# Performance work log

Measured on AMD Instinct MI355X. Metric: run time of the kernel, lower is better.

The kernel has to match this reference:

```python
import jax, jax.numpy as jnp
import numpy as np

K = 49        # k_neighbors
EPS = 1e-5    # BatchNorm2d eps


def setup_inputs() -> dict:
    key = jax.random.key(0)
    ks = jax.random.split(key, 2)
    B, C, M, O = 64, 64, 32, 128
    X = jax.random.normal(ks[0], (B, C, M, M), dtype=jnp.float32)
    # conv1x1 weight (kaiming fan_out) flattened to (O, C); bias init 0
    W = jax.random.normal(ks[1], (O, C), dtype=jnp.float32) * (2.0 / O) ** 0.5
    b = jnp.zeros((O,), jnp.float32)
    gamma = jnp.ones((O,), jnp.float32)
    beta = jnp.zeros((O,), jnp.float32)
    run_mean = jnp.zeros((O,), jnp.float32)
    run_var = jnp.ones((O,), jnp.float32)
    return dict(X=X, W=W, b=b, gamma=gamma, beta=beta,
                run_mean=run_mean, run_var=run_var)


def _knn_aggregate(x):
    """x: (N, C) node features -> D^{-1/2} A D^{-1/2} x for the kNN graph."""
    N = x.shape[0]
    sq = jnp.sum(x * x, axis=1)
    d2 = sq[:, None] + sq[None, :] - 2.0 * (x @ x.T)
    dist = jnp.sqrt(jnp.maximum(d2, 0.0))              # torch.cdist (p=2)
    i = jnp.arange(N)
    dist = dist.at[i, i].set(jnp.inf)                  # fill_diagonal_(inf)
    _, knn = jax.lax.top_k(-dist, K)                   # (N, K) nearest indices
    # topk indices are distinct -> every row degree == K, and the column
    # normalizer uses the col node's row degree (also K), so
    # D^{-1/2} A D^{-1/2} x == mean of gathered neighbors.
    nb = x[knn]                                        # (N, K, C) gather
    return nb.sum(axis=1) / K


def reference(X, W, b, gamma, beta, run_mean, run_var):
    B, C, M, _ = X.shape
    N = M * M
    x = X.reshape(B, C, N).transpose(0, 2, 1)          # (B, N, C) nodes
    Z = jax.vmap(_knn_aggregate)(x)                    # (B, N, C) sparse GCN agg
    # 1x1 conv over the (M, M) grid == per-node linear map
    Fg = jnp.einsum('oc,bnc->bon', W, Z) + b[None, :, None]   # (B, O, N)
    Fg = jax.nn.relu(Fg)
    # BatchNorm2d with running stats (eval mode); Dropout2d is identity in eval
    inv = jax.lax.rsqrt(run_var + EPS)
    Fg = gamma[None, :, None] * (Fg - run_mean[None, :, None]) * inv[None, :, None] + beta[None, :, None]
    return Fg.mean(axis=2)                             # AdaptiveAvgPool2d(1) -> (B, O)
```

## Files before the change

kernel.cpp:

```cpp
#include <hip/hip_runtime.h>
#include <stdint.h>

#define BATCH 64
#define CDIM  64
#define NPTS  1024
#define ODIM  128
#define KNN   49
#define KNNP  52
#define BNEPS 1e-5f
#define ZPAD  72

typedef __attribute__((ext_vector_type(8))) short bf16x8;
typedef __attribute__((ext_vector_type(4))) float f32x4;
typedef union { bf16x8 v; uint32_t d[4]; } bfu;

__device__ __forceinline__ int mbcnt64(unsigned long long m) {
    return __builtin_amdgcn_mbcnt_hi((uint32_t)(m >> 32),
           __builtin_amdgcn_mbcnt_lo((uint32_t)m, 0));
}

__device__ __forceinline__ void bf16_split(float x, uint32_t& h, uint32_t& l) {
    uint32_t u = __float_as_uint(x);
    h = (u + 0x7FFFu + ((u >> 16) & 1u)) >> 16;
    float hf = __uint_as_float(h << 16);
    uint32_t ul = __float_as_uint(x - hf);
    l = (ul + 0x7FFFu + ((ul >> 16) & 1u)) >> 16;
}

#define O_XF   0
#define SZ_XF  (BATCH*64*2*64*8*4)
#define O_SQ   (O_XF + SZ_XF)
#define SZ_SQ  (BATCH*NPTS*4)
#define O_WF   (O_SQ + SZ_SQ)
#define SZ_WF  (2*16*64*16)
#define O_BM   (O_WF + SZ_WF)
#define SZ_BM  (BATCH*NPTS*32*4)
#define O_XFT  (O_BM + SZ_BM)
#define SZ_XFT (BATCH*32*4*64*8*4)
#define WS_NEED ((size_t)(O_XFT + SZ_XFT))

__global__ void gcn_init(const float* __restrict__ gamma, const float* __restrict__ beta,
                         const float* __restrict__ rmean, const float* __restrict__ rvar,
                         float* __restrict__ out) {
    int i = blockIdx.x * 256 + threadIdx.x;
    if (i < BATCH * ODIM) {
        int o = i & (ODIM - 1);
        out[i] = beta[o] - gamma[o] * rmean[o] * rsqrtf(rvar[o] + BNEPS);
    }
}

__global__ __launch_bounds__(256) void k0_split(const float* __restrict__ X,
                                                const float* __restrict__ W,
                                                uint32_t* __restrict__ XF,
                                                float* __restrict__ sq,
                                                uint32_t* __restrict__ XFT,
                                                uint32_t* __restrict__ WFh,
                                                uint32_t* __restrict__ WFl,
                                                const float* __restrict__ gamma,
                                                const float* __restrict__ beta,
                                                const float* __restrict__ rmean,
                                                const float* __restrict__ rvar,
                                                float* __restrict__ out) {
    if (blockIdx.x < 32) {
        int i = blockIdx.x * 256 + threadIdx.x;
        int o = i & (ODIM - 1);
        out[i] = beta[o] - gamma[o] * rmean[o] * rsqrtf(rvar[o] + BNEPS);
    } else if (blockIdx.x < 36) {
        int item = (blockIdx.x - 32) * 256 + threadIdx.x;
        int e = item >> 6, ln = item & 63;
        int nt = e >> 1, kt = e & 1;
        int o = nt * 16 + (ln & 15);
        int kc = kt * 32 + (ln >> 4) * 8;
        const float* wp = W + (size_t)o * CDIM + kc;
        uint32_t h[8], l[8];
#pragma unroll
        for (int jj = 0; jj < 8; jj++) bf16_split(wp[jj], h[jj], l[jj]);
        *(uint4*)&WFh[item * 4] = make_uint4(h[0] | (h[1] << 16), h[2] | (h[3] << 16),
                                             h[4] | (h[5] << 16), h[6] | (h[7] << 16));
        *(uint4*)&WFl[item * 4] = make_uint4(l[0] | (l[1] << 16), l[2] | (l[3] << 16),
                                             l[4] | (l[5] << 16), l[6] | (l[7] << 16));
    }
    const int b    = blockIdx.x >> 4;
    const int g    = blockIdx.x & 15;
    const int wv   = threadIdx.x >> 6;
    const int t16  = g * 4 + wv;
    const int lane = threadIdx.x & 63;
    const int n    = t16 * 16 + (lane & 15);
    const int cg   = lane >> 4;
    const float* Xb = X + (size_t)b * CDIM * NPTS;
    float s = 0.f;
    for (int ks = 0; ks < 2; ks++) {
        uint32_t hi[4], lo[4];
#pragma unroll
        for (int dj = 0; dj < 4; dj++) {
            uint32_t hw[2], lw[2];
#pragma unroll
            for (int e = 0; e < 2; e++) {
                int c = ks * 32 + cg * 8 + dj * 2 + e;
                float x = Xb[(size_t)c * NPTS + n];
                s += x * x;
                bf16_split(x, hw[e], lw[e]);
            }
            hi[dj] = hw[0] | (hw[1] << 16);
            lo[dj] = lw[0] | (lw[1] << 16);
        }
        size_t entry = ((size_t)(b * 64 + t16) * 2 + ks) * 64 + lane;
        uint32_t* p = XF + entry * 8;
        *(uint4*)p       = make_uint4(hi[0], hi[1], hi[2], hi[3]);
        *(uint4*)(p + 4) = make_uint4(lo[0], lo[1], lo[2], lo[3]);
    }
    s += __shfl_xor(s, 16, 64);
    s += __shfl_xor(s, 32, 64);
    if (lane < 16) sq[b * NPTS + n] = s;

#pragma unroll
    for (int sx = 0; sx < 2; sx++) {
        int task = g * 8 + wv * 2 + sx;
        int kt = task >> 2, ct = task & 3;
        int c  = ct * 16 + (lane & 15);
        int n0 = kt * 32 + (lane >> 4) * 8;
        const float* xp = Xb + (size_t)c * NPTS + n0;
        uint32_t h[8], l[8];
#pragma unroll
        for (int j = 0; j < 8; j++) bf16_split(xp[j], h[j], l[j]);
        uint32_t* pp = XFT + ((((size_t)b * 32 + kt) * 4 + ct) * 64 + lane) * 8;
        *(uint4*)pp       = make_uint4(h[0] | (h[1] << 16), h[2] | (h[3] << 16),
                                       h[4] | (h[5] << 16), h[6] | (h[7] << 16));
        *(uint4*)(pp + 4) = make_uint4(l[0] | (l[1] << 16), l[2] | (l[3] << 16),
                                       l[4] | (l[5] << 16), l[6] | (l[7] << 16));
    }
}

__global__ __launch_bounds__(512, 6) void k1_gram_select(const uint32_t* __restrict__ XF,
                                                         const float* __restrict__ sq,
                                                         uint32_t* __restrict__ BM) {
    __shared__ uint32_t s_pk[8 * 1024];
    __shared__ uint32_t s_bm[16][32];
    const int b    = blockIdx.x >> 6;
    const int rt   = blockIdx.x & 63;
    const int wave = threadIdx.x >> 6, lane = threadIdx.x & 63;
    const int q = lane >> 4, l15 = lane & 15;

    bf16x8 ahi[2], alo[2];
#pragma unroll
    for (int ks = 0; ks < 2; ks++) {
        const uint32_t* p = XF + (((size_t)(b * 64 + rt) * 2 + ks) * 64 + lane) * 8;
        ahi[ks] = *(const bf16x8*)p;
        alo[ks] = *(const bf16x8*)(p + 4);
    }
    const float* sqb = sq + b * NPTS;

#pragma unroll
    for (int tt = 0; tt < 8; tt++) {
        const int t16 = wave * 8 + tt;
        f32x4 acc = {0.f, 0.f, 0.f, 0.f};
#pragma unroll
        for (int ks = 0; ks < 2; ks++) {
            const uint32_t* p = XF + (((size_t)(b * 64 + t16) * 2 + ks) * 64 + lane) * 8;
            bf16x8 bhi = *(const bf16x8*)p;
            bf16x8 blo = *(const bf16x8*)(p + 4);
            acc = __builtin_amdgcn_mfma_f32_16x16x32_bf16(ahi[ks], bhi, acc, 0, 0, 0);
            acc = __builtin_amdgcn_mfma_f32_16x16x32_bf16(alo[ks], bhi, acc, 0, 0, 0);
            acc = __builtin_amdgcn_mfma_f32_16x16x32_bf16(ahi[ks], blo, acc, 0, 0, 0);
        }
        const int col  = t16 * 16 + l15;
        const float sqv = sqb[col];
        uint32_t k16[4];
#pragma unroll
        for (int i = 0; i < 4; i++) {
            int row = q * 4 + i;
            float d = fmaf(-2.f, acc[i], sqv);
            if (col == rt * 16 + row) d = __uint_as_float(0x7F800000u);
            uint32_t u = __float_as_uint(d);
            uint32_t key = ((int)u < 0) ? ~u : (u | 0x80000000u);
            k16[i] = key >> 16;
        }
        const int p0 = 2 * q, p1 = 2 * q + 1;
        s_pk[p0 * 1024 + (col ^ ((p0 & 3) << 3))] = k16[0] | (k16[1] << 16);
        s_pk[p1 * 1024 + (col ^ ((p1 & 3) << 3))] = k16[2] | (k16[3] << 16);
    }
    __syncthreads();

    uint32_t k0r[16], k1r[16];
    {
        const int sw = (wave & 3) << 3;
#pragma unroll
        for (int tt = 0; tt < 16; tt++) {
            uint32_t pk = s_pk[wave * 1024 + ((tt * 64 + lane) ^ sw)];
            k0r[tt] = pk & 0xFFFFu;
            k1r[tt] = pk >> 16;
        }
    }

    uint32_t lo0, hi0, lo1, hi1;
    {
        uint32_t lm0 = k0r[0], lm1 = k1r[0];
#pragma unroll
        for (int tt = 1; tt < 16; tt++) {
            lm0 = k0r[tt] < lm0 ? k0r[tt] : lm0;
            lm1 = k1r[tt] < lm1 ? k1r[tt] : lm1;
        }
        uint32_t g0 = lm0, m0 = lm0, g1 = lm1, m1 = lm1;
#pragma unroll
        for (int off = 1; off < 64; off <<= 1) {
            uint32_t a0 = (uint32_t)__shfl_xor((int)g0, off, 64);
            uint32_t b0 = (uint32_t)__shfl_xor((int)m0, off, 64);
            uint32_t a1 = (uint32_t)__shfl_xor((int)g1, off, 64);
            uint32_t b1 = (uint32_t)__shfl_xor((int)m1, off, 64);
            g0 = a0 < g0 ? a0 : g0;  m0 = b0 > m0 ? b0 : m0;
            g1 = a1 < g1 ? a1 : g1;  m1 = b1 > m1 ? b1 : m1;
        }
        lo0 = g0; hi0 = m0;
        lo1 = g1; hi1 = m1;
    }

    for (int it = 0; it < 16; it++) {
        bool a0 = lo0 < hi0, a1 = lo1 < hi1;
        if (!a0 && !a1) break;
        uint32_t mid0 = (lo0 + hi0) >> 1;
        uint32_t mid1 = (lo1 + hi1) >> 1;
        int cnt0 = 0, cnt1 = 0;
#pragma unroll
        for (int tt = 0; tt < 16; tt++) {
            cnt0 += __popcll(__ballot(k0r[tt] <= mid0));
            cnt1 += __popcll(__ballot(k1r[tt] <= mid1));
        }
        if (a0) { if (cnt0 >= KNN) hi0 = mid0; else lo0 = mid0 + 1; }
        if (a1) { if (cnt1 >= KNN) hi1 = mid1; else lo1 = mid1 + 1; }
    }

#pragma unroll
    for (int r = 0; r < 2; r++) {
        const int row = wave * 2 + r;
        const uint32_t vstar = r ? lo1 : lo0;
        const uint32_t* k = r ? k1r : k0r;
        int total_lt = 0;
#pragma unroll
        for (int tt = 0; tt < 16; tt++)
            total_lt += __popcll(__ballot(k[tt] < vstar));
        int base_eq = total_lt;
#pragma unroll
        for (int tt = 0; tt < 16; tt++) {
            bool islt = k[tt] < vstar;
            bool iseq = k[tt] == vstar;
            unsigned long long meq = __ballot(iseq);
            int pos = base_eq + mbcnt64(meq);
            bool sel = islt || (iseq && pos < KNN);
            unsigned long long msel = __ballot(sel);
            if (lane < 2)
                s_bm[row][tt * 2 + lane] = lane ? (uint32_t)(msel >> 32) : (uint32_t)msel;
            base_eq += __popcll(meq);
        }
    }
    __syncthreads();
    if (threadIdx.x < 128) {
        uint32_t* dst = BM + ((size_t)(b * NPTS + rt * 16) * 32);
        *(uint4*)&dst[threadIdx.x * 4] = *(const uint4*)&((const uint32_t*)s_bm)[threadIdx.x * 4];
    }
}

__global__ __launch_bounds__(256) void k2_agg(const uint32_t* __restrict__ XFT,
                                              const uint32_t* __restrict__ BM,
                                              const uint32_t* __restrict__ WFh,
                                              const uint32_t* __restrict__ WFl,
                                              const float* __restrict__ bias,
                                              const float* __restrict__ gamma,
                                              const float* __restrict__ rvar,
                                              float* __restrict__ out) {
    __shared__ uint32_t bmp[128 * 33];
    __shared__ __align__(16) uint16_t ZFh[128 * ZPAD];
    __shared__ __align__(16) uint16_t ZFl[128 * ZPAD];
    __shared__ float red[512];
    const int b = blockIdx.x >> 3, nq = blockIdx.x & 7;
    const int t = threadIdx.x;
    const int wave = t >> 6, lane = t & 63;
    const int q = lane >> 4, l15 = lane & 15;

    {
        const uint32_t* src = BM + ((size_t)(b * NPTS + nq * 128) * 32);
#pragma unroll
        for (int kk = 0; kk < 16; kk++) {
            int idx = kk * 256 + t;
            uint32_t v = src[idx];
            bmp[(idx >> 5) * 33 + (idx & 31)] = v;
        }
    }
    __syncthreads();

    const int ct = wave;
    f32x4 acc[8];
#pragma unroll
    for (int mt = 0; mt < 8; mt++) acc[mt] = (f32x4){0.f, 0.f, 0.f, 0.f};
    for (int kt = 0; kt < 32; kt++) {
        const uint32_t* p = XFT + ((((size_t)b * 32 + kt) * 4 + ct) * 64 + lane) * 8;
        bf16x8 bhi = *(const bf16x8*)p;
        bf16x8 blo = *(const bf16x8*)(p + 4);
#pragma unroll
        for (int mt = 0; mt < 8; mt++) {
            uint32_t byte = (bmp[(mt * 16 + l15) * 33 + kt] >> (q * 8)) & 0xFFu;
            bfu a;
            a.d[0] = ((byte & 1u)  ? 0x3F80u : 0u) | ((byte & 2u)   ? 0x3F800000u : 0u);
            a.d[1] = ((byte & 4u)  ? 0x3F80u : 0u) | ((byte & 8u)   ? 0x3F800000u : 0u);
            a.d[2] = ((byte & 16u) ? 0x3F80u : 0u) | ((byte & 32u)  ? 0x3F800000u : 0u);
            a.d[3] = ((byte & 64u) ? 0x3F80u : 0u) | ((byte & 128u) ? 0x3F800000u : 0u);
            acc[mt] = __builtin_amdgcn_mfma_f32_16x16x32_bf16(a.v, bhi, acc[mt], 0, 0, 0);
            acc[mt] = __builtin_amdgcn_mfma_f32_16x16x32_bf16(a.v, blo, acc[mt], 0, 0, 0);
        }
    }

#pragma unroll
    for (int mt = 0; mt < 8; mt++) {
#pragma unroll
        for (int reg = 0; reg < 4; reg++) {
            int r = mt * 16 + q * 4 + reg;
            int c = ct * 16 + l15;
            uint32_t h, l;
            bf16_split(acc[mt][reg], h, l);
            ZFh[r * ZPAD + c] = (uint16_t)h;
            ZFl[r * ZPAD + c] = (uint16_t)l;
        }
    }
    __syncthreads();

    bf16x8 zah[2][2], zal[2][2];
#pragma unroll
    for (int m2 = 0; m2 < 2; m2++) {
        const int m = (wave * 2 + m2) * 16 + l15;
#pragma unroll
        for (int kt = 0; kt < 2; kt++) {
            const int kb = kt * 32 + q * 8;
            zah[m2][kt] = *(const bf16x8*)&ZFh[m * ZPAD + kb];
            zal[m2][kt] = *(const bf16x8*)&ZFl[m * ZPAD + kb];
        }
    }
    const float inv49 = 1.f / KNN;
    float p[8];
#pragma unroll
    for (int nt = 0; nt < 8; nt++) {
        const int o = nt * 16 + l15;
        bfu wh[2], wl[2];
#pragma unroll
        for (int kt = 0; kt < 2; kt++) {
            const int item = (nt * 2 + kt) * 64 + lane;
            *(uint4*)wh[kt].d = *(const uint4*)&WFh[item * 4];
            *(uint4*)wl[kt].d = *(const uint4*)&WFl[item * 4];
        }
        f32x4 acc0 = {0.f, 0.f, 0.f, 0.f};
        f32x4 acc1 = {0.f, 0.f, 0.f, 0.f};
#pragma unroll
        for (int kt = 0; kt < 2; kt++) {
            acc0 = __builtin_amdgcn_mfma_f32_16x16x32_bf16(zah[0][kt], wh[kt].v, acc0, 0, 0, 0);
            acc0 = __builtin_amdgcn_mfma_f32_16x16x32_bf16(zal[0][kt], wh[kt].v, acc0, 0, 0, 0);
            acc0 = __builtin_amdgcn_mfma_f32_16x16x32_bf16(zah[0][kt], wl[kt].v, acc0, 0, 0, 0);
            acc1 = __builtin_amdgcn_mfma_f32_16x16x32_bf16(zah[1][kt], wh[kt].v, acc1, 0, 0, 0);
            acc1 = __builtin_amdgcn_mfma_f32_16x16x32_bf16(zal[1][kt], wh[kt].v, acc1, 0, 0, 0);
            acc1 = __builtin_amdgcn_mfma_f32_16x16x32_bf16(zah[1][kt], wl[kt].v, acc1, 0, 0, 0);
        }
        const float bo = bias[o];
        float s = 0.f;
#pragma unroll
        for (int reg = 0; reg < 4; reg++) {
            s += fmaxf(fmaf(acc0[reg], inv49, bo), 0.f);
            s += fmaxf(fmaf(acc1[reg], inv49, bo), 0.f);
        }
        p[nt] = s;
    }
#pragma unroll
    for (int nt = 0; nt < 8; nt++) {
        p[nt] += __shfl_xor(p[nt], 16, 64);
        p[nt] += __shfl_xor(p[nt], 32, 64);
    }
    if (lane < 16) {
#pragma unroll
        for (int nt = 0; nt < 8; nt++)
            red[wave * 128 + nt * 16 + l15] = p[nt];
    }
    __syncthreads();
    if (t < 128) {
        float s = red[t] + red[128 + t] + red[256 + t] + red[384 + t];
        float scale = gamma[t] * rsqrtf(rvar[t] + BNEPS) * (1.f / NPTS);
        atomicAdd(&out[b * ODIM + t], s * scale);
    }
}

#define RTILE 8
#define APAD  1028
#define WPAD  132
#define POOLF (64 * WPAD)

__global__ __launch_bounds__(256) void gcn_main(
    const float* __restrict__ X, const float* __restrict__ W,
    const float* __restrict__ bias, const float* __restrict__ gamma,
    const float* __restrict__ rvar, float* __restrict__ out)
{
    __shared__ __align__(16) float s_pool[POOLF];
    __shared__ __align__(16) float s_fstage[4][APAD];
    __shared__ int   s_knn[RTILE][KNN];
    __shared__ float s_z[RTILE][CDIM];

    const int t = threadIdx.x;
    const int b = blockIdx.x >> 7;
    const int rtile = blockIdx.x & 127;
    const int r0 = rtile * RTILE;
    const float* Xb = X + (size_t)b * CDIM * NPTS;

    float acc[RTILE][4];
    float sqv[4];
#pragma unroll
    for (int r = 0; r < RTILE; r++)
#pragma unroll
        for (int u = 0; u < 4; u++) acc[r][u] = 0.f;
#pragma unroll
    for (int u = 0; u < 4; u++) sqv[u] = 0.f;

    for (int ch = 0; ch < 16; ch++) {
        const int c0 = ch * 4;
#pragma unroll
        for (int cc = 0; cc < 4; cc++) {
            float4 v = *(const float4*)(Xb + (size_t)(c0 + cc) * NPTS + 4 * t);
            *(float4*)&s_fstage[cc][4 * t] = v;
        }
        __syncthreads();
#pragma unroll
        for (int cc = 0; cc < 4; cc++) {
            float4 bv4 = *(const float4*)&s_fstage[cc][4 * t];
            float bv[4] = {bv4.x, bv4.y, bv4.z, bv4.w};
#pragma unroll
            for (int u = 0; u < 4; u++) sqv[u] += bv[u] * bv[u];
            const float* arow = Xb + (size_t)(c0 + cc) * NPTS + r0;
            float4 a0 = *(const float4*)(arow);
            float4 a1 = *(const float4*)(arow + 4);
            float av[8] = {a0.x, a0.y, a0.z, a0.w, a1.x, a1.y, a1.z, a1.w};
#pragma unroll
            for (int r = 0; r < RTILE; r++)
#pragma unroll
                for (int u = 0; u < 4; u++) acc[r][u] += av[r] * bv[u];
        }
        __syncthreads();
    }

    float* s_dist = s_pool;
#pragma unroll
    for (int r = 0; r < RTILE; r++) {
        const int rG = r0 + r;
        float d[4];
#pragma unroll
        for (int u = 0; u < 4; u++) {
            float dd = sqv[u] - 2.f * acc[r][u];
            d[u] = (4 * t + u == rG) ? __uint_as_float(0x7F800000u) : dd;
        }
        *(float4*)&s_dist[r * NPTS + 4 * t] = make_float4(d[0], d[1], d[2], d[3]);
    }
    __syncthreads();

    const int wave = t >> 6, lane = t & 63;
    const unsigned long long ltmask = (1ull << lane) - 1ull;
    for (int rr = 0; rr < 2; rr++) {
        const int row = wave * 2 + rr;
        unsigned key[16];
#pragma unroll
        for (int tt = 0; tt < 16; tt++) {
            unsigned u = __float_as_uint(s_dist[row * NPTS + tt * 64 + lane]);
            key[tt] = (u & 0x80000000u) ? ~u : (u | 0x80000000u);
        }
        unsigned lo = 0u, hi = 0xFFFFFFFFu;
        while (lo < hi) {
            unsigned mid = lo + ((hi - lo) >> 1);
            int cnt = 0;
#pragma unroll
            for (int tt = 0; tt < 16; tt++)
                cnt += __popcll(__ballot(key[tt] <= mid));
            if (cnt >= KNN) hi = mid; else lo = mid + 1;
        }
        const unsigned v49 = lo;
        int cntless = 0;
#pragma unroll
        for (int tt = 0; tt < 16; tt++)
            cntless += __popcll(__ballot(key[tt] < v49));
        const int need = KNN - cntless;
        int base = 0, eqtaken = 0;
#pragma unroll
        for (int tt = 0; tt < 16; tt++) {
            bool islt = key[tt] < v49;
            bool iseq = key[tt] == v49;
            unsigned long long meq = __ballot(iseq);
            int eqrank = eqtaken + __popcll(meq & ltmask);
            bool sel = islt || (iseq && (eqrank < need));
            unsigned long long msel = __ballot(sel);
            if (sel) {
                int pos = base + __popcll(msel & ltmask);
                s_knn[row][pos] = tt * 64 + lane;
            }
            base    += __popcll(msel);
            eqtaken += __popcll(meq);
        }
    }
    __syncthreads();

    float* astage = s_pool;
    float* s_redf = (float*)s_fstage;
    const int ar = t >> 5, acc8 = (t & 31) >> 2, ks = t & 3;
    for (int c0 = 0; c0 < CDIM; c0 += 8) {
#pragma unroll
        for (int qq = 0; qq < 8; qq++) {
            int if4 = qq * 256 + t;
            int cc = if4 >> 8, j4 = if4 & 255;
            float4 v = *(const float4*)(Xb + (size_t)(c0 + cc) * NPTS + 4 * j4);
            *(float4*)&astage[cc * APAD + 4 * j4] = v;
        }
        __syncthreads();
        float partial = 0.f;
        for (int k = ks; k < KNN; k += 4)
            partial += astage[acc8 * APAD + s_knn[ar][k]];
        s_redf[t] = partial;
        __syncthreads();
        if (t < 64) {
            int r = t >> 3, cc = t & 7;
            int bi = r * 32 + cc * 4;
            s_z[r][c0 + cc] = s_redf[bi] + s_redf[bi + 1] + s_redf[bi + 2] + s_redf[bi + 3];
        }
        __syncthreads();
    }

    float* wt = s_pool;
#pragma unroll 4
    for (int qq = 0; qq < 32; qq++) {
        int e = qq * 256 + t;
        int o = e >> 6, c = e & 63;
        wt[c * WPAD + o] = W[e];
    }
    __syncthreads();
    const int o = t & 127, rg = t >> 7;
    float facc[4] = {0.f, 0.f, 0.f, 0.f};
    for (int c = 0; c < CDIM; c += 4) {
        float w0 = wt[(c + 0) * WPAD + o], w1 = wt[(c + 1) * WPAD + o];
        float w2 = wt[(c + 2) * WPAD + o], w3 = wt[(c + 3) * WPAD + o];
#pragma unroll
        for (int qq = 0; qq < 4; qq++) {
            float4 zv = *(const float4*)&s_z[rg * 4 + qq][c];
            facc[qq] += w0 * zv.x + w1 * zv.y + w2 * zv.z + w3 * zv.w;
        }
    }
    const float bo = bias[o];
    float rsum = 0.f;
#pragma unroll
    for (int qq = 0; qq < 4; qq++) {
        float f = facc[qq] * (1.f / KNN) + bo;
        rsum += fmaxf(f, 0.f);
    }
    s_redf[t] = rsum;
    __syncthreads();
    if (t < 128) {
        float scale = gamma[t] * rsqrtf(rvar[t] + BNEPS) * (1.f / NPTS);
        atomicAdd(&out[b * ODIM + t], (s_redf[t] + s_redf[t + 128]) * scale);
    }
}

extern "C" void kernel_launch(void* const* d_in, const int* in_sizes, int n_in,
                              void* d_out, int out_size, void* d_ws, size_t ws_size,
                              hipStream_t stream) {
    const float* X     = (const float*)d_in[0];
    const float* W     = (const float*)d_in[1];
    const float* bias  = (const float*)d_in[2];
    const float* gamma = (const float*)d_in[3];
    const float* beta  = (const float*)d_in[4];
    const float* rmean = (const float*)d_in[5];
    const float* rvar  = (const float*)d_in[6];
    float* out = (float*)d_out;

    if (ws_size >= WS_NEED) {
        uint8_t* ws = (uint8_t*)d_ws;
        uint32_t* XF  = (uint32_t*)(ws + O_XF);
        float*    sqw = (float*)(ws + O_SQ);
        uint32_t* WFh = (uint32_t*)(ws + O_WF);
        uint32_t* WFl = WFh + 16 * 64 * 4;
        uint32_t* BM  = (uint32_t*)(ws + O_BM);
        uint32_t* XFT = (uint32_t*)(ws + O_XFT);
        k0_split<<<BATCH * 16, 256, 0, stream>>>(X, W, XF, sqw, XFT, WFh, WFl,
                                                 gamma, beta, rmean, rvar, out);
        k1_gram_select<<<BATCH * 64, 512, 0, stream>>>(XF, sqw, BM);
        k2_agg<<<BATCH * 8, 256, 0, stream>>>(XFT, BM, WFh, WFl, bias, gamma, rvar, out);
    } else {
        gcn_init<<<(BATCH * ODIM + 255) / 256, 256, 0, stream>>>(gamma, beta, rmean, rvar, out);
        gcn_main<<<BATCH * (NPTS / RTILE), 256, 0, stream>>>(X, W, bias, gamma, rvar, out);
    }
}
```

Measured before the change: 230.9 us.

## Double k2_agg block to 512 threads splitting row tiles, prefetch XFT

The aggregation kernel now runs 8 waves per block instead of 4. Each wave handles half the row tiles for its column tile and one 16-row slice in the weight stage, and the final reduction sums eight partials. It also software-prefetches the next k-step's XFT fragments to hide global load latency. The aim is more parallelism and latency hiding in k2, at the cost of each B fragment being loaded by two waves and more shared-memory reduction traffic.

```diff
diff --git a/kernel.cpp b/kernel.cpp
--- a/kernel.cpp
+++ b/kernel.cpp
@@ -259,7 +259,7 @@
     }
 }
 
-__global__ __launch_bounds__(256) void k2_agg(const uint32_t* __restrict__ XFT,
+__global__ __launch_bounds__(512) void k2_agg(const uint32_t* __restrict__ XFT,
                                               const uint32_t* __restrict__ BM,
                                               const uint32_t* __restrict__ WFh,
                                               const uint32_t* __restrict__ WFl,
@@ -270,7 +270,7 @@
     __shared__ uint32_t bmp[128 * 33];
     __shared__ __align__(16) uint16_t ZFh[128 * ZPAD];
     __shared__ __align__(16) uint16_t ZFl[128 * ZPAD];
-    __shared__ float red[512];
+    __shared__ float red[8 * 128];
     const int b = blockIdx.x >> 3, nq = blockIdx.x & 7;
     const int t = threadIdx.x;
     const int wave = t >> 6, lane = t & 63;
@@ -279,59 +279,66 @@
     {
         const uint32_t* src = BM + ((size_t)(b * NPTS + nq * 128) * 32);
 #pragma unroll
-        for (int kk = 0; kk < 16; kk++) {
-            int idx = kk * 256 + t;
+        for (int kk = 0; kk < 8; kk++) {
+            int idx = kk * 512 + t;
             uint32_t v = src[idx];
             bmp[(idx >> 5) * 33 + (idx & 31)] = v;
         }
     }
     __syncthreads();
 
-    const int ct = wave;
-    f32x4 acc[8];
-#pragma unroll
-    for (int mt = 0; mt < 8; mt++) acc[mt] = (f32x4){0.f, 0.f, 0.f, 0.f};
-    for (int kt = 0; kt < 32; kt++) {
-        const uint32_t* p = XFT + ((((size_t)b * 32 + kt) * 4 + ct) * 64 + lane) * 8;
-        bf16x8 bhi = *(const bf16x8*)p;
-        bf16x8 blo = *(const bf16x8*)(p + 4);
-#pragma unroll
-        for (int mt = 0; mt < 8; mt++) {
-            uint32_t byte = (bmp[(mt * 16 + l15) * 33 + kt] >> (q * 8)) & 0xFFu;
-            bfu a;
-            a.d[0] = ((byte & 1u)  ? 0x3F80u : 0u) | ((byte & 2u)   ? 0x3F800000u : 0u);
-            a.d[1] = ((byte & 4u)  ? 0x3F80u : 0u) | ((byte & 8u)   ? 0x3F800000u : 0u);
-            a.d[2] = ((byte & 16u) ? 0x3F80u : 0u) | ((byte & 32u)  ? 0x3F800000u : 0u);
-            a.d[3] = ((byte & 64u) ? 0x3F80u : 0u) | ((byte & 128u) ? 0x3F800000u : 0u);
-            acc[mt] = __builtin_amdgcn_mfma_f32_16x16x32_bf16(a.v, bhi, acc[mt], 0, 0, 0);
-            acc[mt] = __builtin_amdgcn_mfma_f32_16x16x32_bf16(a.v, blo, acc[mt], 0, 0, 0);
-        }
-    }
-
-#pragma unroll
-    for (int mt = 0; mt < 8; mt++) {
+    const int ct = wave & 3, half = wave >> 2;
+    f32x4 acc[4];
+#pragma unroll
+    for (int mtl = 0; mtl < 4; mtl++) acc[mtl] = (f32x4){0.f, 0.f, 0.f, 0.f};
+    {
+        const uint32_t* pb = XFT + (((size_t)b * 32 * 4 + ct) * 64 + lane) * 8;
+        const size_t kstride = (size_t)4 * 64 * 8;
+        bf16x8 bhi = *(const bf16x8*)pb;
+        bf16x8 blo = *(const bf16x8*)(pb + 4);
+        for (int kt = 0; kt < 32; kt++) {
+            bf16x8 nhi, nlo;
+            if (kt < 31) {
+                const uint32_t* pn = pb + (size_t)(kt + 1) * kstride;
+                nhi = *(const bf16x8*)pn;
+                nlo = *(const bf16x8*)(pn + 4);
+            }
+#pragma unroll
+            for (int mtl = 0; mtl < 4; mtl++) {
+                uint32_t byte = (bmp[((half * 4 + mtl) * 16 + l15) * 33 + kt] >> (q * 8)) & 0xFFu;
+                bfu a;
+                a.d[0] = ((byte & 1u)  ? 0x3F80u : 0u) | ((byte & 2u)   ? 0x3F800000u : 0u);
+                a.d[1] = ((byte & 4u)  ? 0x3F80u : 0u) | ((byte & 8u)   ? 0x3F800000u : 0u);
+                a.d[2] = ((byte & 16u) ? 0x3F80u : 0u) | ((byte & 32u)  ? 0x3F800000u : 0u);
+                a.d[3] = ((byte & 64u) ? 0x3F80u : 0u) | ((byte & 128u) ? 0x3F800000u : 0u);
+                acc[mtl] = __builtin_amdgcn_mfma_f32_16x16x32_bf16(a.v, bhi, acc[mtl], 0, 0, 0);
+                acc[mtl] = __builtin_amdgcn_mfma_f32_16x16x32_bf16(a.v, blo, acc[mtl], 0, 0, 0);
+            }
+            bhi = nhi; blo = nlo;
+        }
+    }
+
+#pragma unroll
+    for (int mtl = 0; mtl < 4; mtl++) {
 #pragma unroll
         for (int reg = 0; reg < 4; reg++) {
-            int r = mt * 16 + q * 4 + reg;
+            int r = (half * 4 + mtl) * 16 + q * 4 + reg;
             int c = ct * 16 + l15;
             uint32_t h, l;
-            bf16_split(acc[mt][reg], h, l);
+            bf16_split(acc[mtl][reg], h, l);
             ZFh[r * ZPAD + c] = (uint16_t)h;
             ZFl[r * ZPAD + c] = (uint16_t)l;
         }
     }
     __syncthreads();
 
-    bf16x8 zah[2][2], zal[2][2];
-#pragma unroll
-    for (int m2 = 0; m2 < 2; m2++) {
-        const int m = (wave * 2 + m2) * 16 + l15;
-#pragma unroll
-        for (int kt = 0; kt < 2; kt++) {
-            const int kb = kt * 32 + q * 8;
-            zah[m2][kt] = *(const bf16x8*)&ZFh[m * ZPAD + kb];
-            zal[m2][kt] = *(const bf16x8*)&ZFl[m * ZPAD + kb];
-        }
+    bf16x8 zah[2], zal[2];
+#pragma unroll
+    for (int kt = 0; kt < 2; kt++) {
+        const int m = wave * 16 + l15;
+        const int kb = kt * 32 + q * 8;
+        zah[kt] = *(const bf16x8*)&ZFh[m * ZPAD + kb];
+        zal[kt] = *(const bf16x8*)&ZFl[m * ZPAD + kb];
     }
     const float inv49 = 1.f / KNN;
     float p[8];
@@ -345,30 +352,21 @@
             *(uint4*)wh[kt].d = *(const uint4*)&WFh[item * 4];
             *(uint4*)wl[kt].d = *(const uint4*)&WFl[item * 4];
         }
-        f32x4 acc0 = {0.f, 0.f, 0.f, 0.f};
-        f32x4 acc1 = {0.f, 0.f, 0.f, 0.f};
+        f32x4 accw = {0.f, 0.f, 0.f, 0.f};
 #pragma unroll
         for (int kt = 0; kt < 2; kt++) {
-            acc0 = __builtin_amdgcn_mfma_f32_16x16x32_bf16(zah[0][kt], wh[kt].v, acc0, 0, 0, 0);
-            acc0 = __builtin_amdgcn_mfma_f32_16x16x32_bf16(zal[0][kt], wh[kt].v, acc0, 0, 0, 0);
-            acc0 = __builtin_amdgcn_mfma_f32_16x16x32_bf16(zah[0][kt], wl[kt].v, acc0, 0, 0, 0);
-            acc1 = __builtin_amdgcn_mfma_f32_16x16x32_bf16(zah[1][kt], wh[kt].v, acc1, 0, 0, 0);
-            acc1 = __builtin_amdgcn_mfma_f32_16x16x32_bf16(zal[1][kt], wh[kt].v, acc1, 0, 0, 0);
-            acc1 = __builtin_amdgcn_mfma_f32_16x16x32_bf16(zah[1][kt], wl[kt].v, acc1, 0, 0, 0);
+            accw = __builtin_amdgcn_mfma_f32_16x16x32_bf16(zah[kt], wh[kt].v, accw, 0, 0, 0);
+            accw = __builtin_amdgcn_mfma_f32_16x16x32_bf16(zal[kt], wh[kt].v, accw, 0, 0, 0);
+            accw = __builtin_amdgcn_mfma_f32_16x16x32_bf16(zah[kt], wl[kt].v, accw, 0, 0, 0);
         }
         const float bo = bias[o];
         float s = 0.f;
 #pragma unroll
-        for (int reg = 0; reg < 4; reg++) {
-            s += fmaxf(fmaf(acc0[reg], inv49, bo), 0.f);
-            s += fmaxf(fmaf(acc1[reg], inv49, bo), 0.f);
-        }
+        for (int reg = 0; reg < 4; reg++)
+            s += fmaxf(fmaf(accw[reg], inv49, bo), 0.f);
+        s += __shfl_xor(s, 16, 64);
+        s += __shfl_xor(s, 32, 64);
         p[nt] = s;
-    }
-#pragma unroll
-    for (int nt = 0; nt < 8; nt++) {
-        p[nt] += __shfl_xor(p[nt], 16, 64);
-        p[nt] += __shfl_xor(p[nt], 32, 64);
     }
     if (lane < 16) {
 #pragma unroll
@@ -377,7 +375,9 @@
     }
     __syncthreads();
     if (t < 128) {
-        float s = red[t] + red[128 + t] + red[256 + t] + red[384 + t];
+        float s = 0.f;
+#pragma unroll
+        for (int w = 0; w < 8; w++) s += red[w * 128 + t];
         float scale = gamma[t] * rsqrtf(rvar[t] + BNEPS) * (1.f / NPTS);
         atomicAdd(&out[b * ODIM + t], s * scale);
     }
@@ -579,7 +579,7 @@
         k0_split<<<BATCH * 16, 256, 0, stream>>>(X, W, XF, sqw, XFT, WFh, WFl,
                                                  gamma, beta, rmean, rvar, out);
         k1_gram_select<<<BATCH * 64, 512, 0, stream>>>(XF, sqw, BM);
-        k2_agg<<<BATCH * 8, 256, 0, stream>>>(XFT, BM, WFh, WFl, bias, gamma, rvar, out);
+        k2_agg<<<BATCH * 8, 512, 0, stream>>>(XFT, BM, WFh, WFl, bias, gamma, rvar, out);
     } else {
         gcn_init<<<(BATCH * ODIM + 255) / 256, 256, 0, stream>>>(gamma, beta, rmean, rvar, out);
         gcn_main<<<BATCH * (NPTS / RTILE), 256, 0, stream>>>(X, W, bias, gamma, rvar, out);
```

New measurement: 233.5 us. No clear change (+1.2%).
